# Performance work log

Hardware: AMD Instinct MI355X
Metric: run time of the kernel (lower is better)

Reference implementation:

```python
import jax, jax.numpy as jnp
import numpy as np

H = 512; W = 512; C = 32; E = 32; NH = 2; HD = 16; B = 4; N = 50000
SHIFTS = jnp.array([[0, 0], [-1, 0], [1, 0], [0, 1], [-1, 1], [1, 1], [0, -1], [-1, -1], [1, -1]], dtype=jnp.int32)


def setup_inputs() -> dict:
    key = jax.random.key(0)
    ks = jax.random.split(key, 12)

    def coords(k):
        # unique BEV cells per sample -> well-defined coord->index lookup
        flat = jax.random.permutation(k, H * W)[:N]
        return jnp.stack([flat // W, flat % W], axis=-1).astype(jnp.int32)

    li_coors = jnp.stack([coords(jax.random.fold_in(ks[0], b)) for b in range(B)])
    ra_coors = jnp.stack([coords(jax.random.fold_in(ks[1], b)) for b in range(B)])
    li_feats = jax.random.normal(ks[2], (B, N, C), jnp.float32)
    ra_feats = jax.random.normal(ks[3], (B, N, C), jnp.float32)
    s = 0.1
    return {
        "li_feats": li_feats, "li_coors": li_coors,
        "ra_feats": ra_feats, "ra_coors": ra_coors,
        "w_qkv1": jax.random.normal(ks[4], (3 * E, E), jnp.float32) * s,
        "b_qkv1": jax.random.normal(ks[5], (3 * E,), jnp.float32) * s,
        "w_out1": jax.random.normal(ks[6], (E, E), jnp.float32) * s,
        "b_out1": jax.random.normal(ks[7], (E,), jnp.float32) * s,
        "w_qkv2": jax.random.normal(ks[8], (3 * E, E), jnp.float32) * s,
        "b_qkv2": jax.random.normal(ks[9], (3 * E,), jnp.float32) * s,
        "w_out2": jax.random.normal(ks[10], (E, E), jnp.float32) * s,
        "b_out2": jax.random.normal(ks[11], (E,), jnp.float32) * s,
    }


def _mha(q, kv, w_qkv, b_qkv, w_out, b_out):
    # q: [N,1,E], kv: [N,9,E]; torch MultiheadAttention (eval, dropout off)
    wq, wk, wv = jnp.split(w_qkv, 3, axis=0)
    bq, bk, bv = jnp.split(b_qkv, 3)
    n = q.shape[0]
    Q = (q @ wq.T + bq).reshape(n, 1, NH, HD)
    K = (kv @ wk.T + bk).reshape(n, 9, NH, HD)
    V = (kv @ wv.T + bv).reshape(n, 9, NH, HD)
    s = jnp.einsum('nqhd,nkhd->nhqk', Q, K) / jnp.sqrt(jnp.float32(HD))
    a = jax.nn.softmax(s, axis=-1)
    o = jnp.einsum('nhqk,nkhd->nqhd', a, V).reshape(n, E)
    return o @ w_out.T + b_out


def _gather_keys(q_coor, kv_coor, kv_feat):
    # dense grid lookup: BEV cell -> voxel index in kv (-1 if empty)
    nk = kv_coor.shape[0]
    grid = jnp.full((H * W,), -1, jnp.int32).at[kv_coor[:, 0] * W + kv_coor[:, 1]].set(
        jnp.arange(nk, dtype=jnp.int32))
    sh = q_coor[:, None, :] + SHIFTS[None]  # [N,9,2]
    valid = (sh[..., 0] >= 0) & (sh[..., 0] < H) & (sh[..., 1] >= 0) & (sh[..., 1] < W)
    flat = jnp.clip(sh[..., 0], 0, H - 1) * W + jnp.clip(sh[..., 1], 0, W - 1)
    idx = jnp.where(valid, grid[flat], -1)  # [N,9]
    keys = jnp.where((idx >= 0)[..., None], kv_feat[jnp.clip(idx, 0)], 0.0)
    return keys  # [N,9,C]


def _scatter(feat, coor):
    # PointPillarsScatter: place [N,C] voxel feats into dense [C,H,W] canvas
    flat = coor[:, 0] * W + coor[:, 1]
    return jnp.zeros((C, H * W), feat.dtype).at[:, flat].set(feat.T).reshape(C, H, W)


def _branch(q_feat, q_coor, kv_feat, kv_coor, w_qkv, b_qkv, w_out, b_out):
    keys = _gather_keys(q_coor, kv_coor, kv_feat)
    out = _mha(q_feat[:, None, :], keys, w_qkv, b_qkv, w_out, b_out)
    return _scatter(q_feat + out, q_coor)


def reference(li_feats, li_coors, ra_feats, ra_coors,
              w_qkv1, b_qkv1, w_out1, b_out1,
              w_qkv2, b_qkv2, w_out2, b_out2):
    vb = jax.vmap(_branch, in_axes=(0, 0, 0, 0, None, None, None, None))
    li_img = vb(li_feats, li_coors, ra_feats, ra_coors, w_qkv1, b_qkv1, w_out1, b_out1)
    ra_img = vb(ra_feats, ra_coors, li_feats, li_coors, w_qkv2, b_qkv2, w_out2, b_out2)
    return (li_img, ra_img)  # each [B, C, H, W]
```

## Files before the change

### kernel.cpp

```cpp
#include <hip/hip_runtime.h>

#define HH 512
#define WW 512
#define HWC (HH * WW)
#define NV 50000
#define NB 4
#define NR (NB * NV)
#define NQ (2 * NR)
#define KVROWS (NR + 1)

typedef unsigned int uint32;

static __device__ __forceinline__ float4 ld4(const float* p) {
    return *reinterpret_cast<const float4*>(p);
}
static __device__ __forceinline__ uint32 bf16rne(float x) {
    uint32 u = __float_as_uint(x);
    return (u + 0x7FFFu + ((u >> 16) & 1u)) >> 16;
}

static __device__ __forceinline__ float red16(float x) {
    float t;
    t = __int_as_float(__builtin_amdgcn_update_dpp(0, __float_as_int(x), 0xB1, 0xF, 0xF, true));
    x += t;
    t = __int_as_float(__builtin_amdgcn_update_dpp(0, __float_as_int(x), 0x4E, 0xF, 0xF, true));
    x += t;
    t = __int_as_float(__builtin_amdgcn_update_dpp(0, __float_as_int(x), 0x141, 0xF, 0xF, true));
    x += t;
    t = __int_as_float(__builtin_amdgcn_update_dpp(0, __float_as_int(x), 0x140, 0xF, 0xF, true));
    x += t;
    return x;
}

__global__ void k_fill(int4* __restrict__ p) {
    const int total = 2 * NB * HWC / 4;
    const int stride = gridDim.x * blockDim.x;
    const int4 v = make_int4(-1, -1, -1, -1);
    for (int i = blockIdx.x * blockDim.x + threadIdx.x; i < total; i += stride)
        p[i] = v;
}

__global__ void k_grid(const int* __restrict__ li_coors, const int* __restrict__ ra_coors,
                       int* __restrict__ grids) {
    int t = blockIdx.x * blockDim.x + threadIdx.x;
    if (t >= NQ) return;
    int set = t / NR;
    int r2 = t - set * NR;
    int b = r2 / NV;
    int n = r2 - b * NV;
    const int* co = (set == 0 ? li_coors : ra_coors) + (size_t)(b * NV + n) * 2;
    grids[(set * NB + b) * HWC + co[0] * WW + co[1]] = n;
}

__launch_bounds__(256)
__global__ void k_proj_kv(const float* __restrict__ li_feats, const float* __restrict__ ra_feats,
                          const float* __restrict__ w_qkv1, const float* __restrict__ b_qkv1,
                          const float* __restrict__ w_qkv2, const float* __restrict__ b_qkv2,
                          uint32* __restrict__ KV) {
    const int f = blockIdx.y;
    const float* feats = f ? ra_feats : li_feats;
    const float* wkv_g = f ? w_qkv1 : w_qkv2;
    const float* bkv_g = f ? b_qkv1 : b_qkv2;

    __shared__ float xs[4][2][64];
    const int wave = threadIdx.x >> 6;
    const int l    = threadIdx.x & 63;
    const int h    = l >> 5;
    const int j    = l & 31;

    const int gw = blockIdx.x * 4 + wave;
    const int gs = gridDim.x * 4;

    int r0 = gw * 2;
    float xreg = feats[(size_t)r0 * 32 + l];

    float4 wk[8], wv[8];
#pragma unroll
    for (int i = 0; i < 8; ++i) {
        wk[i] = ld4(wkv_g + (32 + j) * 32 + i * 4);
        wv[i] = ld4(wkv_g + (64 + j) * 32 + i * 4);
    }
    const float bk = bkv_g[32 + j], bv = bkv_g[64 + j];

    uint32* KVb = KV + (size_t)(f ^ 1) * KVROWS * 32;

    if (blockIdx.x == 0 && threadIdx.x < 32)
        KVb[(size_t)NR * 32 + threadIdx.x] = bf16rne(bk) | (bf16rne(bv) << 16);

    int cur = 0;
    while (r0 < NR) {
        xs[wave][cur][l] = xreg;
        const int rn = r0 + gs * 2;
        if (rn < NR) xreg = feats[(size_t)rn * 32 + l];

        const float* xp = &xs[wave][cur][h * 32];
        float ak = bk, av = bv;
#pragma unroll
        for (int i = 0; i < 8; ++i) {
            float4 x = *reinterpret_cast<const float4*>(xp + i * 4);
            ak += x.x * wk[i].x + x.y * wk[i].y + x.z * wk[i].z + x.w * wk[i].w;
            av += x.x * wv[i].x + x.y * wv[i].y + x.z * wv[i].z + x.w * wv[i].w;
        }
        KVb[(size_t)(r0 + h) * 32 + j] = bf16rne(ak) | (bf16rne(av) << 16);
        r0 = rn;
        cur ^= 1;
    }
}

__global__ void k_nbr(const int* __restrict__ li_coors, const int* __restrict__ ra_coors,
                      const int* __restrict__ grids, int* __restrict__ nbr) {
    int q = blockIdx.x * 256 + threadIdx.x;
    if (q >= NQ) return;
    int br  = (q >= NR) ? 1 : 0;
    int rem = q - br * NR;
    int b   = rem / NV;
    const int* qc = br ? ra_coors : li_coors;
    const int* kvgrid = grids + ((br ^ 1) * NB + b) * HWC;
    const int2 rc = *reinterpret_cast<const int2*>(qc + (size_t)rem * 2);

    const int drs[9] = {0, -1, 1, 0, -1, 1, 0, -1, 1};
    const int dcs[9] = {0, 0, 0, 1, 1, 1, -1, -1, -1};
    const int base = b * NV;
    int v[9];
#pragma unroll
    for (int k = 0; k < 9; ++k) {
        int rr = rc.x + drs[k], cc = rc.y + dcs[k];
        bool valid = ((unsigned)rr < HH) & ((unsigned)cc < WW);
        int raw = kvgrid[valid ? rr * WW + cc : 0];
        int id = valid ? raw : -1;
        v[k] = (id >= 0 ? base + id : NR) * 128;
    }
    int4* np = reinterpret_cast<int4*>(nbr + (size_t)q * 12);
    np[0] = make_int4(v[0], v[1], v[2], v[3]);
    np[1] = make_int4(v[4], v[5], v[6], v[7]);
    np[2] = make_int4(v[8], 0, 0, 0);
}

__launch_bounds__(256)
__global__ void k_attn(const int* __restrict__ nbr,
                       const float* __restrict__ li_feats, const float* __restrict__ ra_feats,
                       const float* __restrict__ w_qkv1, const float* __restrict__ b_qkv1,
                       const float* __restrict__ w_out1, const float* __restrict__ b_out1,
                       const float* __restrict__ w_qkv2, const float* __restrict__ b_qkv2,
                       const float* __restrict__ w_out2, const float* __restrict__ b_out2,
                       const uint32* __restrict__ KV, float* __restrict__ res) {
    __shared__ float xs[8][4][32];
    __shared__ float os[8][4][32];
    const int g = threadIdx.x >> 5;
    const int j = threadIdx.x & 31;
    const int q0 = (blockIdx.x * 8 + g) * 4;
    const int br  = (q0 >= NR) ? 1 : 0;
    const int rem = q0 - br * NR;
    const float* feats = br ? ra_feats : li_feats;
    const float* wqkv  = br ? w_qkv2 : w_qkv1;
    const float* bqkv  = br ? b_qkv2 : b_qkv1;
    const float* wout  = br ? w_out2 : w_out1;
    const float* bout  = br ? b_out2 : b_out1;
    const char* KVbr = (const char*)(KV + (size_t)br * KVROWS * 32);

    int4 a0[4], a1[4], a2[4];
#pragma unroll
    for (int u = 0; u < 4; ++u) {
        const int4* np = reinterpret_cast<const int4*>(nbr + (size_t)(q0 + u) * 12);
        a0[u] = np[0]; a1[u] = np[1]; a2[u] = np[2];
    }

    float fr[4];
#pragma unroll
    for (int u = 0; u < 4; ++u) {
        fr[u] = feats[(size_t)(rem + u) * 32 + j];
        xs[g][u][j] = fr[u];
    }

    const int joff = j * 4;
    uint32 kvw[4][9];
#pragma unroll
    for (int u = 0; u < 4; ++u) {
        int off[9] = {a0[u].x, a0[u].y, a0[u].z, a0[u].w,
                      a1[u].x, a1[u].y, a1[u].z, a1[u].w, a2[u].x};
#pragma unroll
        for (int k = 0; k < 9; ++k)
            kvw[u][k] = *reinterpret_cast<const uint32*>(KVbr + (size_t)(unsigned)(off[k] + joff));
    }

    const float bq = bqkv[j];
    float Qf[4] = {bq, bq, bq, bq};
#pragma unroll
    for (int i = 0; i < 8; ++i) {
        float4 w = ld4(wqkv + j * 32 + i * 4);
#pragma unroll
        for (int u = 0; u < 4; ++u) {
            float4 x = *reinterpret_cast<const float4*>(&xs[g][u][i * 4]);
            Qf[u] += x.x * w.x + x.y * w.y + x.z * w.z + x.w * w.w;
        }
    }
    const float SC = 0.25f * 1.44269504f;
#pragma unroll
    for (int u = 0; u < 4; ++u) Qf[u] *= SC;

#pragma unroll
    for (int u = 0; u < 4; ++u) {
        float sum = 0.f, o = 0.f;
#pragma unroll
        for (int k = 0; k < 9; ++k) {
            float kk = __uint_as_float(kvw[u][k] << 16);
            float e = exp2f(red16(Qf[u] * kk));
            float vv = __uint_as_float(kvw[u][k] & 0xFFFF0000u);
            sum += e;
            o += e * vv;
        }
        os[g][u][j] = o / sum;
    }

    const float bo = bout[j];
    float outv[4] = {bo, bo, bo, bo};
#pragma unroll
    for (int i = 0; i < 8; ++i) {
        float4 w = ld4(wout + j * 32 + i * 4);
#pragma unroll
        for (int u = 0; u < 4; ++u) {
            float4 x = *reinterpret_cast<const float4*>(&os[g][u][i * 4]);
            outv[u] += x.x * w.x + x.y * w.y + x.z * w.z + x.w * w.w;
        }
    }
#pragma unroll
    for (int u = 0; u < 4; ++u)
        res[(size_t)(q0 + u) * 32 + j] = fr[u] + outv[u];
}

__launch_bounds__(256)
__global__ void k_densify(const int* __restrict__ grids, const float* __restrict__ res,
                          float* __restrict__ out) {
    int t = blockIdx.x * 256 + threadIdx.x;
    int plane = t >> 18;
    int s = t & (HWC - 1);
    int gidx = grids[t];
    float4 v[8];
    if (gidx >= 0) {
        const float* rp = res + ((size_t)plane * NV + gidx) * 32;
#pragma unroll
        for (int i = 0; i < 8; ++i) v[i] = ld4(rp + i * 4);
    } else {
#pragma unroll
        for (int i = 0; i < 8; ++i) v[i] = make_float4(0.f, 0.f, 0.f, 0.f);
    }
    float* ob = out + (size_t)plane * 32 * HWC + s;
#pragma unroll
    for (int i = 0; i < 8; ++i) {
        ob[(size_t)(4 * i + 0) * HWC] = v[i].x;
        ob[(size_t)(4 * i + 1) * HWC] = v[i].y;
        ob[(size_t)(4 * i + 2) * HWC] = v[i].z;
        ob[(size_t)(4 * i + 3) * HWC] = v[i].w;
    }
}

extern "C" void kernel_launch(void* const* d_in, const int* in_sizes, int n_in,
                              void* d_out, int out_size, void* d_ws, size_t ws_size,
                              hipStream_t stream) {
    const float* li_feats = (const float*)d_in[0];
    const int*   li_coors = (const int*)d_in[1];
    const float* ra_feats = (const float*)d_in[2];
    const int*   ra_coors = (const int*)d_in[3];
    const float* w_qkv1 = (const float*)d_in[4];
    const float* b_qkv1 = (const float*)d_in[5];
    const float* w_out1 = (const float*)d_in[6];
    const float* b_out1 = (const float*)d_in[7];
    const float* w_qkv2 = (const float*)d_in[8];
    const float* b_qkv2 = (const float*)d_in[9];
    const float* w_out2 = (const float*)d_in[10];
    const float* b_out2 = (const float*)d_in[11];
    float* out = (float*)d_out;

    char* ws = (char*)d_ws;
    size_t off = 0;
    int*    grids = (int*)(ws + off);    off += (size_t)2 * NB * HWC * 4;
    uint32* KV    = (uint32*)(ws + off); off += (size_t)2 * KVROWS * 32 * 4;
    float*  res   = (float*)(ws + off);  off += (size_t)NQ * 32 * 4;
    int*    nbr   = (int*)(ws + off);    off += (size_t)NQ * 12 * 4;

    k_fill<<<2048, 256, 0, stream>>>((int4*)grids);

    k_grid<<<(NQ + 255) / 256, 256, 0, stream>>>(li_coors, ra_coors, grids);

    k_proj_kv<<<dim3(3200, 2), 256, 0, stream>>>(
        li_feats, ra_feats, w_qkv1, b_qkv1, w_qkv2, b_qkv2, KV);

    k_nbr<<<(NQ + 255) / 256, 256, 0, stream>>>(li_coors, ra_coors, grids, nbr);

    k_attn<<<NQ / 32, 256, 0, stream>>>(
        nbr, li_feats, ra_feats,
        w_qkv1, b_qkv1, w_out1, b_out1,
        w_qkv2, b_qkv2, w_out2, b_out2,
        KV, res);

    k_densify<<<(2 * NB * HWC) / 256, 256, 0, stream>>>(grids, res, out);
}
```

Baseline: 287.5 us.

## Use packed FP32 FMAs in attention projections and nontemporal stores in densify

The attention kernel's shared-memory staging is transposed to [feature][query] so four queries' inputs load as one float4. The Q and output projections then use inline v_pk_fma_f32 with op_sel to update two queries per instruction. Separately, the densify kernel writes the large dense output canvas with nontemporal stores to avoid polluting the cache. The inline asm ties the code to packed-FP32 support and may limit compiler scheduling; the transposed LDS layout could change bank-conflict behavior.

```diff
diff --git a/kernel.cpp b/kernel.cpp
--- a/kernel.cpp
+++ b/kernel.cpp
@@ -17,6 +17,15 @@
 static __device__ __forceinline__ uint32 bf16rne(float x) {
     uint32 u = __float_as_uint(x);
     return (u + 0x7FFFu + ((u >> 16) & 1u)) >> 16;
+}
+
+static __device__ __forceinline__ void pk_fma_lo(float2& a, float2 w, float2 x) {
+    asm("v_pk_fma_f32 %0, %1, %2, %0 op_sel:[0,0,0] op_sel_hi:[0,1,1]"
+        : "+v"(a) : "v"(w), "v"(x));
+}
+static __device__ __forceinline__ void pk_fma_hi(float2& a, float2 w, float2 x) {
+    asm("v_pk_fma_f32 %0, %1, %2, %0 op_sel:[1,0,0] op_sel_hi:[1,1,1]"
+        : "+v"(a) : "v"(w), "v"(x));
 }
 
 static __device__ __forceinline__ float red16(float x) {
@@ -144,8 +153,8 @@
                        const float* __restrict__ w_qkv2, const float* __restrict__ b_qkv2,
                        const float* __restrict__ w_out2, const float* __restrict__ b_out2,
                        const uint32* __restrict__ KV, float* __restrict__ res) {
-    __shared__ float xs[8][4][32];
-    __shared__ float os[8][4][32];
+    __shared__ float xs[8][32][4];
+    __shared__ float os[8][32][4];
     const int g = threadIdx.x >> 5;
     const int j = threadIdx.x & 31;
     const int q0 = (blockIdx.x * 8 + g) * 4;
@@ -165,12 +174,12 @@
         a0[u] = np[0]; a1[u] = np[1]; a2[u] = np[2];
     }
 
-    float fr[4];
-#pragma unroll
-    for (int u = 0; u < 4; ++u) {
-        fr[u] = feats[(size_t)(rem + u) * 32 + j];
-        xs[g][u][j] = fr[u];
-    }
+    float4 frv;
+    frv.x = feats[(size_t)(rem + 0) * 32 + j];
+    frv.y = feats[(size_t)(rem + 1) * 32 + j];
+    frv.z = feats[(size_t)(rem + 2) * 32 + j];
+    frv.w = feats[(size_t)(rem + 3) * 32 + j];
+    *reinterpret_cast<float4*>(xs[g][j]) = frv;
 
     const int joff = j * 4;
     uint32 kvw[4][9];
@@ -184,20 +193,29 @@
     }
 
     const float bq = bqkv[j];
-    float Qf[4] = {bq, bq, bq, bq};
+    float2 q01 = make_float2(bq, bq), q23 = make_float2(bq, bq);
 #pragma unroll
     for (int i = 0; i < 8; ++i) {
         float4 w = ld4(wqkv + j * 32 + i * 4);
-#pragma unroll
-        for (int u = 0; u < 4; ++u) {
-            float4 x = *reinterpret_cast<const float4*>(&xs[g][u][i * 4]);
-            Qf[u] += x.x * w.x + x.y * w.y + x.z * w.z + x.w * w.w;
-        }
+        float2 w01 = make_float2(w.x, w.y);
+        float2 w23 = make_float2(w.z, w.w);
+        float4 x0 = *reinterpret_cast<const float4*>(xs[g][i * 4 + 0]);
+        float4 x1 = *reinterpret_cast<const float4*>(xs[g][i * 4 + 1]);
+        float4 x2 = *reinterpret_cast<const float4*>(xs[g][i * 4 + 2]);
+        float4 x3 = *reinterpret_cast<const float4*>(xs[g][i * 4 + 3]);
+        pk_fma_lo(q01, w01, make_float2(x0.x, x0.y));
+        pk_fma_lo(q23, w01, make_float2(x0.z, x0.w));
+        pk_fma_hi(q01, w01, make_float2(x1.x, x1.y));
+        pk_fma_hi(q23, w01, make_float2(x1.z, x1.w));
+        pk_fma_lo(q01, w23, make_float2(x2.x, x2.y));
+        pk_fma_lo(q23, w23, make_float2(x2.z, x2.w));
+        pk_fma_hi(q01, w23, make_float2(x3.x, x3.y));
+        pk_fma_hi(q23, w23, make_float2(x3.z, x3.w));
     }
     const float SC = 0.25f * 1.44269504f;
-#pragma unroll
-    for (int u = 0; u < 4; ++u) Qf[u] *= SC;
-
+    float Qf[4] = {q01.x * SC, q01.y * SC, q23.x * SC, q23.y * SC};
+
+    float4 ov;
 #pragma unroll
     for (int u = 0; u < 4; ++u) {
         float sum = 0.f, o = 0.f;
@@ -209,23 +227,36 @@
             sum += e;
             o += e * vv;
         }
-        os[g][u][j] = o / sum;
-    }
+        float r = o / sum;
+        if (u == 0) ov.x = r; else if (u == 1) ov.y = r;
+        else if (u == 2) ov.z = r; else ov.w = r;
+    }
+    *reinterpret_cast<float4*>(os[g][j]) = ov;
 
     const float bo = bout[j];
-    float outv[4] = {bo, bo, bo, bo};
+    float2 o01 = make_float2(bo, bo), o23 = make_float2(bo, bo);
 #pragma unroll
     for (int i = 0; i < 8; ++i) {
         float4 w = ld4(wout + j * 32 + i * 4);
-#pragma unroll
-        for (int u = 0; u < 4; ++u) {
-            float4 x = *reinterpret_cast<const float4*>(&os[g][u][i * 4]);
-            outv[u] += x.x * w.x + x.y * w.y + x.z * w.z + x.w * w.w;
-        }
-    }
-#pragma unroll
-    for (int u = 0; u < 4; ++u)
-        res[(size_t)(q0 + u) * 32 + j] = fr[u] + outv[u];
+        float2 w01 = make_float2(w.x, w.y);
+        float2 w23 = make_float2(w.z, w.w);
+        float4 x0 = *reinterpret_cast<const float4*>(os[g][i * 4 + 0]);
+        float4 x1 = *reinterpret_cast<const float4*>(os[g][i * 4 + 1]);
+        float4 x2 = *reinterpret_cast<const float4*>(os[g][i * 4 + 2]);
+        float4 x3 = *reinterpret_cast<const float4*>(os[g][i * 4 + 3]);
+        pk_fma_lo(o01, w01, make_float2(x0.x, x0.y));
+        pk_fma_lo(o23, w01, make_float2(x0.z, x0.w));
+        pk_fma_hi(o01, w01, make_float2(x1.x, x1.y));
+        pk_fma_hi(o23, w01, make_float2(x1.z, x1.w));
+        pk_fma_lo(o01, w23, make_float2(x2.x, x2.y));
+        pk_fma_lo(o23, w23, make_float2(x2.z, x2.w));
+        pk_fma_hi(o01, w23, make_float2(x3.x, x3.y));
+        pk_fma_hi(o23, w23, make_float2(x3.z, x3.w));
+    }
+    res[(size_t)(q0 + 0) * 32 + j] = frv.x + o01.x;
+    res[(size_t)(q0 + 1) * 32 + j] = frv.y + o01.y;
+    res[(size_t)(q0 + 2) * 32 + j] = frv.z + o23.x;
+    res[(size_t)(q0 + 3) * 32 + j] = frv.w + o23.y;
 }
 
 __launch_bounds__(256)
@@ -247,10 +278,10 @@
     float* ob = out + (size_t)plane * 32 * HWC + s;
 #pragma unroll
     for (int i = 0; i < 8; ++i) {
-        ob[(size_t)(4 * i + 0) * HWC] = v[i].x;
-        ob[(size_t)(4 * i + 1) * HWC] = v[i].y;
-        ob[(size_t)(4 * i + 2) * HWC] = v[i].z;
-        ob[(size_t)(4 * i + 3) * HWC] = v[i].w;
+        __builtin_nontemporal_store(v[i].x, ob + (size_t)(4 * i + 0) * HWC);
+        __builtin_nontemporal_store(v[i].y, ob + (size_t)(4 * i + 1) * HWC);
+        __builtin_nontemporal_store(v[i].z, ob + (size_t)(4 * i + 2) * HWC);
+        __builtin_nontemporal_store(v[i].w, ob + (size_t)(4 * i + 3) * HWC);
     }
 }
 
```

New measurement: 354.5 us. +23.3%, slower.
